# Performance work log

Hardware: AMD Instinct MI355X
Metric: run time of the kernel (lower is better)

## Reference

```python
import jax, jax.numpy as jnp
import numpy as np

NEG_INF = -1e30  # stand-in for float('-inf') that is safe under softmax


def setup_inputs() -> dict:
    key = jax.random.key(0)
    k1, k2, k3, k4 = jax.random.split(key, 4)
    B, T, C, H = 4, 4096, 1024, 128
    x = jax.random.normal(k1, (B, T, C), dtype=jnp.float32)
    # nn.Linear(n_emb, head_size, bias=False): store as [C, H] so y = x @ W
    Wk = jax.random.normal(k2, (C, H), dtype=jnp.float32) * (C ** -0.5)
    Wq = jax.random.normal(k3, (C, H), dtype=jnp.float32) * (C ** -0.5)
    Wv = jax.random.normal(k4, (C, H), dtype=jnp.float32) * (C ** -0.5)
    return {"x": x, "Wk": Wk, "Wq": Wq, "Wv": Wv}


def reference(x, Wk, Wq, Wv):
    B, T, C = x.shape
    k = x @ Wk  # [B, T, H]
    q = x @ Wq  # [B, T, H]
    v = x @ Wv  # [B, T, H]
    # Faithful to original: wei = k @ q^T, scaled by C**-0.5 (C = n_emb)
    wei = jnp.einsum('bih,bjh->bij', k, q) * (C ** -0.5)  # [B, T, T]
    causal = jnp.tril(jnp.ones((T, T), dtype=bool))
    wei = jnp.where(causal, wei, NEG_INF)
    wei = jax.nn.softmax(wei, axis=-1)
    out = jnp.einsum('bij,bjh->bih', wei, v)  # [B, T, H]
    return out
```

## Files before the change

kernel.cpp:

```cpp
#include <hip/hip_runtime.h>
#include <hip/hip_bf16.h>

#define T_SEQ 4096
#define NBATCH 4
#define C_EMB 1024
#define H_DIM 128
#define M_ROWS (NBATCH * T_SEQ)
#define SPLIT 4

typedef __bf16 bf16x8 __attribute__((ext_vector_type(8)));
typedef float  floatx4 __attribute__((ext_vector_type(4)));

__device__ __forceinline__ ushort f2bf(float f) {
    __hip_bfloat16 h = __float2bfloat16(f);
    return *reinterpret_cast<ushort*>(&h);
}
__device__ __forceinline__ float bf2f(ushort u) {
    unsigned int v = ((unsigned int)u) << 16;
    return *reinterpret_cast<float*>(&v);
}
__device__ __forceinline__ uint4 pack8(const float4& a, const float4& b) {
    __hip_bfloat162 h0 = __float22bfloat162_rn(make_float2(a.x, a.y));
    __hip_bfloat162 h1 = __float22bfloat162_rn(make_float2(a.z, a.w));
    __hip_bfloat162 h2 = __float22bfloat162_rn(make_float2(b.x, b.y));
    __hip_bfloat162 h3 = __float22bfloat162_rn(make_float2(b.z, b.w));
    uint4 r;
    r.x = *reinterpret_cast<unsigned int*>(&h0);
    r.y = *reinterpret_cast<unsigned int*>(&h1);
    r.z = *reinterpret_cast<unsigned int*>(&h2);
    r.w = *reinterpret_cast<unsigned int*>(&h3);
    return r;
}
__device__ __forceinline__ void gld16(const ushort* g, ushort* l) {
    __builtin_amdgcn_global_load_lds(
        (const __attribute__((address_space(1))) unsigned int*)(g),
        (__attribute__((address_space(3))) unsigned int*)(l),
        16, 0, 0);
}

__global__ __launch_bounds__(256) void transpose_w(
    const float* __restrict__ Wk, const float* __restrict__ Wq,
    const float* __restrict__ Wv, ushort* __restrict__ wt) {
    const int z = blockIdx.y;
    const float* W = (z == 0) ? Wk : (z == 1) ? Wq : Wv;
    ushort* Wtz = wt + (size_t)z * H_DIM * C_EMB;
    int linear = blockIdx.x * 256 + threadIdx.x;
    int n  = linear >> 7;
    int k0 = (linear & 127) << 3;
    ushort tmp[8];
#pragma unroll
    for (int j = 0; j < 8; ++j)
        tmp[j] = f2bf(W[(size_t)(k0 + j) * H_DIM + n]);
    uint4 pk;
    pk.x = (unsigned int)tmp[0] | ((unsigned int)tmp[1] << 16);
    pk.y = (unsigned int)tmp[2] | ((unsigned int)tmp[3] << 16);
    pk.z = (unsigned int)tmp[4] | ((unsigned int)tmp[5] << 16);
    pk.w = (unsigned int)tmp[6] | ((unsigned int)tmp[7] << 16);
    *reinterpret_cast<uint4*>(Wtz + (size_t)n * C_EMB + k0) = pk;
}

__global__ __launch_bounds__(512, 1) void qkv_gemm(
    const float* __restrict__ x, const ushort* __restrict__ wt,
    ushort* __restrict__ kqv) {
    const int m0 = blockIdx.x * 64;

    __shared__ ushort As[2][64 * 64];
    __shared__ ushort Bs[2][384 * 64];

    const int tid  = threadIdx.x;
    const int lane = tid & 63;
    const int wave = tid >> 6;
    const int l15  = lane & 15;
    const int quad = lane >> 4;
    const int mg   = (wave >> 1) * 16;
    const int nb   = (wave & 1) * 12;

    floatx4 acc[12];
#pragma unroll
    for (int nj = 0; nj < 12; ++nj) acc[nj] = floatx4{0.f, 0.f, 0.f, 0.f};

    const int ar = tid >> 3;
    const int ac = tid & 7;
    const int chp = ac ^ (ar & 7);
    const float* xrow = x + (size_t)(m0 + ar) * C_EMB + ac * 8;

    float4 xa = *reinterpret_cast<const float4*>(xrow);
    float4 xb = *reinterpret_cast<const float4*>(xrow + 4);
#pragma unroll
    for (int i = 0; i < 6; ++i) {
        int rbase = wave * 48 + i * 8;
        int row = rbase + (lane >> 3);
        int chg = (lane & 7) ^ (row & 7);
        gld16(wt + (size_t)row * C_EMB + chg * 8, Bs[0] + rbase * 64);
    }
    *reinterpret_cast<uint4*>(As[0] + ar * 64 + chp * 8) = pack8(xa, xb);
    __syncthreads();
    xa = *reinterpret_cast<const float4*>(xrow + 64);
    xb = *reinterpret_cast<const float4*>(xrow + 68);

    for (int kt = 0; kt < 16; ++kt) {
        const int cur = kt & 1;

        if (kt < 15) {
#pragma unroll
            for (int i = 0; i < 6; ++i) {
                int rbase = wave * 48 + i * 8;
                int row = rbase + (lane >> 3);
                int chg = (lane & 7) ^ (row & 7);
                gld16(wt + (size_t)row * C_EMB + (kt + 1) * 64 + chg * 8,
                      Bs[cur ^ 1] + rbase * 64);
            }
            *reinterpret_cast<uint4*>(As[cur ^ 1] + ar * 64 + chp * 8) = pack8(xa, xb);
        }
        if (kt < 14) {
            const float* nsrc = xrow + (kt + 2) * 64;
            xa = *reinterpret_cast<const float4*>(nsrc);
            xb = *reinterpret_cast<const float4*>(nsrc + 4);
        }

#pragma unroll
        for (int kk = 0; kk < 2; ++kk) {
            bf16x8 a = *reinterpret_cast<const bf16x8*>(
                As[cur] + (mg + l15) * 64 + ((4 * kk + quad) ^ (l15 & 7)) * 8);
#pragma unroll
            for (int nj = 0; nj < 12; ++nj) {
                int brow = (nb + nj) * 16 + l15;
                bf16x8 b = *reinterpret_cast<const bf16x8*>(
                    Bs[cur] + brow * 64 + ((4 * kk + quad) ^ (brow & 7)) * 8);
                acc[nj] = __builtin_amdgcn_mfma_f32_16x16x32_bf16(a, b, acc[nj], 0, 0, 0);
            }
        }

        __syncthreads();
    }

    const int rowb = m0 + mg + quad * 4;
#pragma unroll
    for (int nj = 0; nj < 12; ++nj) {
        int gcol = (nb + nj) * 16 + l15;
        int z = gcol >> 7;
        int cz = gcol & 127;
        if (z < 2) {
            const float scale = (z == 0) ? 0.03125f : 1.0f;
            ushort* outz = kqv + (size_t)z * M_ROWS * H_DIM;
#pragma unroll
            for (int r = 0; r < 4; ++r)
                outz[(size_t)(rowb + r) * H_DIM + cz] = f2bf(acc[nj][r] * scale);
        } else {
            ushort* vt = kqv + (size_t)2 * M_ROWS * H_DIM;
            int bb   = rowb >> 12;
            int tloc = rowb & (T_SEQ - 1);
            ushort4 pk;
            pk.x = f2bf(acc[nj][0]);
            pk.y = f2bf(acc[nj][1]);
            pk.z = f2bf(acc[nj][2]);
            pk.w = f2bf(acc[nj][3]);
            *reinterpret_cast<ushort4*>(
                vt + ((size_t)(bb * H_DIM + cz) << 12) + tloc) = pk;
        }
    }
}

#define P_STRIDE 72
__global__ __launch_bounds__(256, 3) void flash_chunk(
    const ushort* __restrict__ kqv, ushort* __restrict__ partO,
    float* __restrict__ partML) {
    const int it = blockIdx.x >> 2;
    const int c  = blockIdx.x & 3;
    if (c > it) return;
    const int b  = blockIdx.y;
    const int i0 = it * 64;

    const ushort* Qg = kqv + (size_t)b * T_SEQ * H_DIM;
    const ushort* Kg = kqv + (size_t)M_ROWS * H_DIM + (size_t)b * T_SEQ * H_DIM;
    const ushort* Vt = kqv + (size_t)2 * M_ROWS * H_DIM + (size_t)b * H_DIM * T_SEQ;

    __shared__ ushort Ks[64 * 128];
    __shared__ ushort Vs[128 * 64];
    __shared__ ushort Ps[4][16 * P_STRIDE];

    const int tid  = threadIdx.x;
    const int lane = tid & 63;
    const int wave = tid >> 6;
    const int l15  = lane & 15;
    const int quad = lane >> 4;

    bf16x8 q[4];
    {
        const ushort* qrow = Qg + (size_t)(i0 + wave * 16 + l15) * H_DIM + quad * 8;
#pragma unroll
        for (int kk = 0; kk < 4; ++kk)
            q[kk] = *reinterpret_cast<const bf16x8*>(qrow + kk * 32);
    }

    float m_i[4], l_i[4];
#pragma unroll
    for (int r = 0; r < 4; ++r) { m_i[r] = -1e30f; l_i[r] = 0.f; }
    floatx4 o[8];
#pragma unroll
    for (int nh = 0; nh < 8; ++nh) o[nh] = floatx4{0.f, 0.f, 0.f, 0.f};

    ushort* Pw = Ps[wave];

    for (int jt = c; jt <= it; jt += SPLIT) {
        const int j0 = jt * 64;
        __syncthreads();
#pragma unroll
        for (int i = 0; i < 4; ++i) {
            int row = wave * 16 + i * 4 + (lane >> 4);
            int chg = (lane & 15) ^ (row & 15);
            gld16(Kg + (size_t)(j0 + row) * H_DIM + chg * 8,
                  Ks + (wave * 16 + i * 4) * 128);
        }
#pragma unroll
        for (int i = 0; i < 4; ++i) {
            int row = wave * 32 + i * 8 + (lane >> 3);
            int chg = (lane & 7) ^ (row & 7);
            gld16(Vt + (size_t)row * T_SEQ + j0 + chg * 8,
                  Vs + (wave * 32 + i * 8) * 64);
        }
        __syncthreads();

        floatx4 s[4];
#pragma unroll
        for (int ni = 0; ni < 4; ++ni) s[ni] = floatx4{0.f, 0.f, 0.f, 0.f};
#pragma unroll
        for (int kk = 0; kk < 4; ++kk)
#pragma unroll
            for (int ni = 0; ni < 4; ++ni) {
                bf16x8 kb = *reinterpret_cast<const bf16x8*>(
                    Ks + (ni * 16 + l15) * 128 + ((4 * kk + quad) ^ l15) * 8);
                s[ni] = __builtin_amdgcn_mfma_f32_16x16x32_bf16(q[kk], kb, s[ni], 0, 0, 0);
            }

        if (jt == it) {
            int ii = i0 + wave * 16 + quad * 4;
#pragma unroll
            for (int ni = 0; ni < 4; ++ni) {
                int j = j0 + ni * 16 + l15;
#pragma unroll
                for (int r = 0; r < 4; ++r)
                    if (j > ii + r) s[ni][r] = -1e30f;
            }
        }

        float alpha[4], rs[4];
#pragma unroll
        for (int r = 0; r < 4; ++r) {
            float v = fmaxf(fmaxf(s[0][r], s[1][r]), fmaxf(s[2][r], s[3][r]));
#pragma unroll
            for (int off = 8; off >= 1; off >>= 1)
                v = fmaxf(v, __shfl_xor(v, off, 64));
            float mn = fmaxf(m_i[r], v);
            alpha[r] = __expf(m_i[r] - mn);
            m_i[r] = mn;
            rs[r] = 0.f;
        }
#pragma unroll
        for (int ni = 0; ni < 4; ++ni)
#pragma unroll
            for (int r = 0; r < 4; ++r) {
                float p = __expf(s[ni][r] - m_i[r]);
                rs[r] += p;
                Pw[(quad * 4 + r) * P_STRIDE + ni * 16 + l15] = f2bf(p);
            }
#pragma unroll
        for (int r = 0; r < 4; ++r) {
            float v = rs[r];
#pragma unroll
            for (int off = 8; off >= 1; off >>= 1)
                v += __shfl_xor(v, off, 64);
            l_i[r] = l_i[r] * alpha[r] + v;
        }
#pragma unroll
        for (int nh = 0; nh < 8; ++nh)
#pragma unroll
            for (int r = 0; r < 4; ++r) o[nh][r] *= alpha[r];

#pragma unroll
        for (int kp = 0; kp < 2; ++kp) {
            bf16x8 a = *reinterpret_cast<const bf16x8*>(
                Pw + l15 * P_STRIDE + kp * 32 + quad * 8);
#pragma unroll
            for (int nh = 0; nh < 8; ++nh) {
                bf16x8 vb = *reinterpret_cast<const bf16x8*>(
                    Vs + (nh * 16 + l15) * 64 + ((4 * kp + quad) ^ (l15 & 7)) * 8);
                o[nh] = __builtin_amdgcn_mfma_f32_16x16x32_bf16(a, vb, o[nh], 0, 0, 0);
            }
        }
    }

    const int idx = ((b * 64 + it) << 2) + c;
    ushort* po = partO + (size_t)idx * 64 * 128;
#pragma unroll
    for (int nh = 0; nh < 8; ++nh)
#pragma unroll
        for (int r = 0; r < 4; ++r) {
            int row = wave * 16 + quad * 4 + r;
            po[(size_t)row * 128 + nh * 16 + l15] = f2bf(o[nh][r]);
        }
    if (l15 == 0) {
        float* ml = partML + (size_t)idx * 128;
#pragma unroll
        for (int r = 0; r < 4; ++r) {
            int row = wave * 16 + quad * 4 + r;
            ml[row]      = m_i[r];
            ml[64 + row] = l_i[r];
        }
    }
}

__global__ __launch_bounds__(256) void combine(
    const ushort* __restrict__ partO, const float* __restrict__ partML,
    float* __restrict__ out) {
    const int it = blockIdx.x, b = blockIdx.y;
    const int count = min(SPLIT, it + 1);
    const int tid = threadIdx.x;
    const int row = tid >> 2;
    const int cg  = (tid & 3) * 32;
    const int base = (b * 64 + it) << 2;

    float m_c[SPLIT], l_c[SPLIT];
    float M = -1e30f;
    for (int cc = 0; cc < count; ++cc) {
        const float* ml = partML + (size_t)(base + cc) * 128;
        m_c[cc] = ml[row];
        l_c[cc] = ml[64 + row];
        M = fmaxf(M, m_c[cc]);
    }
    float L = 0.f, w[SPLIT];
    for (int cc = 0; cc < count; ++cc) {
        w[cc] = __expf(m_c[cc] - M);
        L += w[cc] * l_c[cc];
    }

    float acc[32];
#pragma unroll
    for (int j = 0; j < 32; ++j) acc[j] = 0.f;
    for (int cc = 0; cc < count; ++cc) {
        const ushort* po = partO + (size_t)(base + cc) * 8192 + (size_t)row * 128 + cg;
        float wc = w[cc];
#pragma unroll
        for (int g = 0; g < 4; ++g) {
            uint4 v = *reinterpret_cast<const uint4*>(po + g * 8);
            const ushort* pv = reinterpret_cast<const ushort*>(&v);
#pragma unroll
            for (int e = 0; e < 8; ++e)
                acc[g * 8 + e] += wc * bf2f(pv[e]);
        }
    }
    float invL = 1.0f / L;
    float* op = out + ((size_t)b * T_SEQ + it * 64 + row) * H_DIM + cg;
#pragma unroll
    for (int g = 0; g < 8; ++g) {
        float4 v;
        v.x = acc[g * 4 + 0] * invL;
        v.y = acc[g * 4 + 1] * invL;
        v.z = acc[g * 4 + 2] * invL;
        v.w = acc[g * 4 + 3] * invL;
        *reinterpret_cast<float4*>(op + g * 4) = v;
    }
}

extern "C" void kernel_launch(void* const* d_in, const int* in_sizes, int n_in,
                              void* d_out, int out_size, void* d_ws, size_t ws_size,
                              hipStream_t stream) {
    const float* x  = (const float*)d_in[0];
    const float* Wk = (const float*)d_in[1];
    const float* Wq = (const float*)d_in[2];
    const float* Wv = (const float*)d_in[3];

    ushort* kqv    = (ushort*)d_ws;
    ushort* wt     = kqv + (size_t)3 * M_ROWS * H_DIM;
    ushort* partO  = wt + (size_t)3 * H_DIM * C_EMB;
    float*  partML = (float*)(partO + (size_t)1024 * 64 * 128);

    transpose_w<<<dim3(64, 3), 256, 0, stream>>>(Wk, Wq, Wv, wt);
    qkv_gemm<<<dim3(256), 512, 0, stream>>>(x, wt, kqv);
    flash_chunk<<<dim3(64 * SPLIT, NBATCH), 256, 0, stream>>>(kqv, partO, partML);
    combine<<<dim3(64, NBATCH), 256, 0, stream>>>(partO, partML, (float*)d_out);
}
```

Baseline: 181.0 us.

## Use 128-row query tiles with 8 waves per block, heavy tiles first

The flash kernel now has each 512-thread block handle 128 query rows (8 waves) instead of 64, so every loaded K/V tile in shared memory serves twice as many query rows. Blocks are ordered so the longest causal rows get scheduled first. Waves whose rows lie entirely before a key tile skip its compute, and the causal mask applies whenever the tile crosses the diagonal. The partial-output layout and the combine indexing change to match. The cost is fewer blocks, higher per-block resource use, and some idle waves on diagonal tiles.

```diff
diff --git a/kernel.cpp b/kernel.cpp
--- a/kernel.cpp
+++ b/kernel.cpp
@@ -162,14 +162,15 @@
 }
 
 #define P_STRIDE 72
-__global__ __launch_bounds__(256, 3) void flash_chunk(
+__global__ __launch_bounds__(512, 2) void flash_chunk(
     const ushort* __restrict__ kqv, ushort* __restrict__ partO,
     float* __restrict__ partML) {
-    const int it = blockIdx.x >> 2;
-    const int c  = blockIdx.x & 3;
-    if (c > it) return;
+    const int it2 = 31 - (blockIdx.x >> 2);
+    const int c   = blockIdx.x & 3;
+    const int maxjt = 2 * it2 + 1;
+    if (c > maxjt) return;
     const int b  = blockIdx.y;
-    const int i0 = it * 64;
+    const int i0 = it2 * 128;
 
     const ushort* Qg = kqv + (size_t)b * T_SEQ * H_DIM;
     const ushort* Kg = kqv + (size_t)M_ROWS * H_DIM + (size_t)b * T_SEQ * H_DIM;
@@ -177,17 +178,18 @@
 
     __shared__ ushort Ks[64 * 128];
     __shared__ ushort Vs[128 * 64];
-    __shared__ ushort Ps[4][16 * P_STRIDE];
+    __shared__ ushort Ps[8][16 * P_STRIDE];
 
     const int tid  = threadIdx.x;
     const int lane = tid & 63;
     const int wave = tid >> 6;
     const int l15  = lane & 15;
     const int quad = lane >> 4;
+    const int wrow0 = i0 + wave * 16;
 
     bf16x8 q[4];
     {
-        const ushort* qrow = Qg + (size_t)(i0 + wave * 16 + l15) * H_DIM + quad * 8;
+        const ushort* qrow = Qg + (size_t)(wrow0 + l15) * H_DIM + quad * 8;
 #pragma unroll
         for (int kk = 0; kk < 4; ++kk)
             q[kk] = *reinterpret_cast<const bf16x8*>(qrow + kk * 32);
@@ -202,24 +204,26 @@
 
     ushort* Pw = Ps[wave];
 
-    for (int jt = c; jt <= it; jt += SPLIT) {
+    for (int jt = c; jt <= maxjt; jt += SPLIT) {
         const int j0 = jt * 64;
         __syncthreads();
 #pragma unroll
-        for (int i = 0; i < 4; ++i) {
-            int row = wave * 16 + i * 4 + (lane >> 4);
+        for (int i = 0; i < 2; ++i) {
+            int rb = wave * 8 + i * 4;
+            int row = rb + (lane >> 4);
             int chg = (lane & 15) ^ (row & 15);
-            gld16(Kg + (size_t)(j0 + row) * H_DIM + chg * 8,
-                  Ks + (wave * 16 + i * 4) * 128);
-        }
-#pragma unroll
-        for (int i = 0; i < 4; ++i) {
-            int row = wave * 32 + i * 8 + (lane >> 3);
+            gld16(Kg + (size_t)(j0 + row) * H_DIM + chg * 8, Ks + rb * 128);
+        }
+#pragma unroll
+        for (int i = 0; i < 2; ++i) {
+            int rb = wave * 16 + i * 8;
+            int row = rb + (lane >> 3);
             int chg = (lane & 7) ^ (row & 7);
-            gld16(Vt + (size_t)row * T_SEQ + j0 + chg * 8,
-                  Vs + (wave * 32 + i * 8) * 64);
+            gld16(Vt + (size_t)row * T_SEQ + j0 + chg * 8, Vs + rb * 64);
         }
         __syncthreads();
+
+        if (j0 > wrow0 + 15) continue;
 
         floatx4 s[4];
 #pragma unroll
@@ -233,8 +237,8 @@
                 s[ni] = __builtin_amdgcn_mfma_f32_16x16x32_bf16(q[kk], kb, s[ni], 0, 0, 0);
             }
 
-        if (jt == it) {
-            int ii = i0 + wave * 16 + quad * 4;
+        if (j0 + 63 > wrow0) {
+            int ii = wrow0 + quad * 4;
 #pragma unroll
             for (int ni = 0; ni < 4; ++ni) {
                 int j = j0 + ni * 16 + l15;
@@ -290,8 +294,8 @@
         }
     }
 
-    const int idx = ((b * 64 + it) << 2) + c;
-    ushort* po = partO + (size_t)idx * 64 * 128;
+    const int idx = ((b * 32 + it2) << 2) + c;
+    ushort* po = partO + (size_t)idx * 128 * 128;
 #pragma unroll
     for (int nh = 0; nh < 8; ++nh)
 #pragma unroll
@@ -300,12 +304,12 @@
             po[(size_t)row * 128 + nh * 16 + l15] = f2bf(o[nh][r]);
         }
     if (l15 == 0) {
-        float* ml = partML + (size_t)idx * 128;
+        float* ml = partML + (size_t)idx * 256;
 #pragma unroll
         for (int r = 0; r < 4; ++r) {
             int row = wave * 16 + quad * 4 + r;
-            ml[row]      = m_i[r];
-            ml[64 + row] = l_i[r];
+            ml[row]       = m_i[r];
+            ml[128 + row] = l_i[r];
         }
     }
 }
@@ -314,18 +318,21 @@
     const ushort* __restrict__ partO, const float* __restrict__ partML,
     float* __restrict__ out) {
     const int it = blockIdx.x, b = blockIdx.y;
-    const int count = min(SPLIT, it + 1);
+    const int it2  = it >> 1;
+    const int roff = (it & 1) * 64;
+    const int count = min(SPLIT, 2 * it2 + 2);
     const int tid = threadIdx.x;
     const int row = tid >> 2;
     const int cg  = (tid & 3) * 32;
-    const int base = (b * 64 + it) << 2;
+    const int base = ((b * 32 + it2) << 2);
+    const int row128 = roff + row;
 
     float m_c[SPLIT], l_c[SPLIT];
     float M = -1e30f;
     for (int cc = 0; cc < count; ++cc) {
-        const float* ml = partML + (size_t)(base + cc) * 128;
-        m_c[cc] = ml[row];
-        l_c[cc] = ml[64 + row];
+        const float* ml = partML + (size_t)(base + cc) * 256;
+        m_c[cc] = ml[row128];
+        l_c[cc] = ml[128 + row128];
         M = fmaxf(M, m_c[cc]);
     }
     float L = 0.f, w[SPLIT];
@@ -338,7 +345,7 @@
 #pragma unroll
     for (int j = 0; j < 32; ++j) acc[j] = 0.f;
     for (int cc = 0; cc < count; ++cc) {
-        const ushort* po = partO + (size_t)(base + cc) * 8192 + (size_t)row * 128 + cg;
+        const ushort* po = partO + (size_t)(base + cc) * 16384 + (size_t)row128 * 128 + cg;
         float wc = w[cc];
 #pragma unroll
         for (int g = 0; g < 4; ++g) {
@@ -373,10 +380,10 @@
     ushort* kqv    = (ushort*)d_ws;
     ushort* wt     = kqv + (size_t)3 * M_ROWS * H_DIM;
     ushort* partO  = wt + (size_t)3 * H_DIM * C_EMB;
-    float*  partML = (float*)(partO + (size_t)1024 * 64 * 128);
+    float*  partML = (float*)(partO + (size_t)512 * 128 * 128);
 
     transpose_w<<<dim3(64, 3), 256, 0, stream>>>(Wk, Wq, Wv, wt);
     qkv_gemm<<<dim3(256), 512, 0, stream>>>(x, wt, kqv);
-    flash_chunk<<<dim3(64 * SPLIT, NBATCH), 256, 0, stream>>>(kqv, partO, partML);
+    flash_chunk<<<dim3(32 * SPLIT, NBATCH), 512, 0, stream>>>(kqv, partO, partML);
     combine<<<dim3(64, NBATCH), 256, 0, stream>>>(partO, partML, (float*)d_out);
 }
```

New measurement: 191.2 us. +5.6%, slower.

## Retile QKV GEMM to 128x192 blocks and swizzle P buffer in attention

Applied to the files above, without the earlier changes.

The QKV projection GEMM now uses 128-row by 192-column tiles across a 2D grid, so each block stages half the weight columns and twice the x rows. Each wave owns 16 rows by all 192 columns. The aim is to reduce redundant weight staging per output and raise occupancy with launch bounds of 4. The attention kernel replaces the padded P scratch stride with an XOR-swizzled 64-wide layout, which cuts LDS usage and allows 4 blocks per CU. The cost is that the x tile is now re-read by two column blocks, and register pressure rises under the higher occupancy bounds.

```diff
diff --git a/kernel.cpp b/kernel.cpp
--- a/kernel.cpp
+++ b/kernel.cpp
@@ -59,21 +59,21 @@
     *reinterpret_cast<uint4*>(Wtz + (size_t)n * C_EMB + k0) = pk;
 }
 
-__global__ __launch_bounds__(512, 1) void qkv_gemm(
+__global__ __launch_bounds__(512, 4) void qkv_gemm(
     const float* __restrict__ x, const ushort* __restrict__ wt,
     ushort* __restrict__ kqv) {
-    const int m0 = blockIdx.x * 64;
-
-    __shared__ ushort As[2][64 * 64];
-    __shared__ ushort Bs[2][384 * 64];
+    const int m0 = blockIdx.x * 128;
+    const int cb = blockIdx.y * 192;
+
+    __shared__ ushort As[2][128 * 64];
+    __shared__ ushort Bs[2][192 * 64];
 
     const int tid  = threadIdx.x;
     const int lane = tid & 63;
     const int wave = tid >> 6;
     const int l15  = lane & 15;
     const int quad = lane >> 4;
-    const int mg   = (wave >> 1) * 16;
-    const int nb   = (wave & 1) * 12;
+    const int mg   = wave * 16;
 
     floatx4 acc[12];
 #pragma unroll
@@ -82,40 +82,50 @@
     const int ar = tid >> 3;
     const int ac = tid & 7;
     const int chp = ac ^ (ar & 7);
-    const float* xrow = x + (size_t)(m0 + ar) * C_EMB + ac * 8;
-
-    float4 xa = *reinterpret_cast<const float4*>(xrow);
-    float4 xb = *reinterpret_cast<const float4*>(xrow + 4);
-#pragma unroll
-    for (int i = 0; i < 6; ++i) {
-        int rbase = wave * 48 + i * 8;
+    const float* xr0 = x + (size_t)(m0 + ar) * C_EMB + ac * 8;
+    const float* xr1 = xr0 + (size_t)64 * C_EMB;
+
+    float4 xa0 = *reinterpret_cast<const float4*>(xr0);
+    float4 xb0 = *reinterpret_cast<const float4*>(xr0 + 4);
+    float4 xa1 = *reinterpret_cast<const float4*>(xr1);
+    float4 xb1 = *reinterpret_cast<const float4*>(xr1 + 4);
+#pragma unroll
+    for (int i = 0; i < 3; ++i) {
+        int rbase = wave * 24 + i * 8;
         int row = rbase + (lane >> 3);
         int chg = (lane & 7) ^ (row & 7);
-        gld16(wt + (size_t)row * C_EMB + chg * 8, Bs[0] + rbase * 64);
-    }
-    *reinterpret_cast<uint4*>(As[0] + ar * 64 + chp * 8) = pack8(xa, xb);
+        gld16(wt + (size_t)(cb + row) * C_EMB + chg * 8, Bs[0] + rbase * 64);
+    }
+    *reinterpret_cast<uint4*>(As[0] + ar * 64 + chp * 8)        = pack8(xa0, xb0);
+    *reinterpret_cast<uint4*>(As[0] + (ar + 64) * 64 + chp * 8) = pack8(xa1, xb1);
     __syncthreads();
-    xa = *reinterpret_cast<const float4*>(xrow + 64);
-    xb = *reinterpret_cast<const float4*>(xrow + 68);
+    xa0 = *reinterpret_cast<const float4*>(xr0 + 64);
+    xb0 = *reinterpret_cast<const float4*>(xr0 + 68);
+    xa1 = *reinterpret_cast<const float4*>(xr1 + 64);
+    xb1 = *reinterpret_cast<const float4*>(xr1 + 68);
 
     for (int kt = 0; kt < 16; ++kt) {
         const int cur = kt & 1;
 
         if (kt < 15) {
 #pragma unroll
-            for (int i = 0; i < 6; ++i) {
-                int rbase = wave * 48 + i * 8;
+            for (int i = 0; i < 3; ++i) {
+                int rbase = wave * 24 + i * 8;
                 int row = rbase + (lane >> 3);
                 int chg = (lane & 7) ^ (row & 7);
-                gld16(wt + (size_t)row * C_EMB + (kt + 1) * 64 + chg * 8,
+                gld16(wt + (size_t)(cb + row) * C_EMB + (kt + 1) * 64 + chg * 8,
                       Bs[cur ^ 1] + rbase * 64);
             }
-            *reinterpret_cast<uint4*>(As[cur ^ 1] + ar * 64 + chp * 8) = pack8(xa, xb);
+            *reinterpret_cast<uint4*>(As[cur ^ 1] + ar * 64 + chp * 8)        = pack8(xa0, xb0);
+            *reinterpret_cast<uint4*>(As[cur ^ 1] + (ar + 64) * 64 + chp * 8) = pack8(xa1, xb1);
         }
         if (kt < 14) {
-            const float* nsrc = xrow + (kt + 2) * 64;
-            xa = *reinterpret_cast<const float4*>(nsrc);
-            xb = *reinterpret_cast<const float4*>(nsrc + 4);
+            const float* n0 = xr0 + (kt + 2) * 64;
+            const float* n1 = xr1 + (kt + 2) * 64;
+            xa0 = *reinterpret_cast<const float4*>(n0);
+            xb0 = *reinterpret_cast<const float4*>(n0 + 4);
+            xa1 = *reinterpret_cast<const float4*>(n1);
+            xb1 = *reinterpret_cast<const float4*>(n1 + 4);
         }
 
 #pragma unroll
@@ -124,9 +134,9 @@
                 As[cur] + (mg + l15) * 64 + ((4 * kk + quad) ^ (l15 & 7)) * 8);
 #pragma unroll
             for (int nj = 0; nj < 12; ++nj) {
-                int brow = (nb + nj) * 16 + l15;
+                int brow = nj * 16 + l15;
                 bf16x8 b = *reinterpret_cast<const bf16x8*>(
-                    Bs[cur] + brow * 64 + ((4 * kk + quad) ^ (brow & 7)) * 8);
+                    Bs[cur] + brow * 64 + ((4 * kk + quad) ^ (l15 & 7)) * 8);
                 acc[nj] = __builtin_amdgcn_mfma_f32_16x16x32_bf16(a, b, acc[nj], 0, 0, 0);
             }
         }
@@ -137,7 +147,7 @@
     const int rowb = m0 + mg + quad * 4;
 #pragma unroll
     for (int nj = 0; nj < 12; ++nj) {
-        int gcol = (nb + nj) * 16 + l15;
+        int gcol = cb + nj * 16 + l15;
         int z = gcol >> 7;
         int cz = gcol & 127;
         if (z < 2) {
@@ -161,8 +171,7 @@
     }
 }
 
-#define P_STRIDE 72
-__global__ __launch_bounds__(256, 3) void flash_chunk(
+__global__ __launch_bounds__(256, 4) void flash_chunk(
     const ushort* __restrict__ kqv, ushort* __restrict__ partO,
     float* __restrict__ partML) {
     const int it = blockIdx.x >> 2;
@@ -177,7 +186,7 @@
 
     __shared__ ushort Ks[64 * 128];
     __shared__ ushort Vs[128 * 64];
-    __shared__ ushort Ps[4][16 * P_STRIDE];
+    __shared__ ushort Ps[4][16 * 64];
 
     const int tid  = threadIdx.x;
     const int lane = tid & 63;
@@ -262,7 +271,9 @@
             for (int r = 0; r < 4; ++r) {
                 float p = __expf(s[ni][r] - m_i[r]);
                 rs[r] += p;
-                Pw[(quad * 4 + r) * P_STRIDE + ni * 16 + l15] = f2bf(p);
+                int prow = quad * 4 + r;
+                int pc8  = (ni * 2 + (l15 >> 3)) ^ (prow & 7);
+                Pw[prow * 64 + pc8 * 8 + (l15 & 7)] = f2bf(p);
             }
 #pragma unroll
         for (int r = 0; r < 4; ++r) {
@@ -280,7 +291,7 @@
 #pragma unroll
         for (int kp = 0; kp < 2; ++kp) {
             bf16x8 a = *reinterpret_cast<const bf16x8*>(
-                Pw + l15 * P_STRIDE + kp * 32 + quad * 8);
+                Pw + l15 * 64 + ((kp * 4 + quad) ^ (l15 & 7)) * 8);
 #pragma unroll
             for (int nh = 0; nh < 8; ++nh) {
                 bf16x8 vb = *reinterpret_cast<const bf16x8*>(
@@ -376,7 +387,7 @@
     float*  partML = (float*)(partO + (size_t)1024 * 64 * 128);
 
     transpose_w<<<dim3(64, 3), 256, 0, stream>>>(Wk, Wq, Wv, wt);
-    qkv_gemm<<<dim3(256), 512, 0, stream>>>(x, wt, kqv);
+    qkv_gemm<<<dim3(128, 2), 512, 0, stream>>>(x, wt, kqv);
     flash_chunk<<<dim3(64 * SPLIT, NBATCH), 256, 0, stream>>>(kqv, partO, partML);
     combine<<<dim3(64, NBATCH), 256, 0, stream>>>(partO, partML, (float*)d_out);
 }
```

After: 209.0 us. 1.15x slower.
